# Kernel optimization log

Hardware: AMD Instinct MI355X
Metric: run time of the kernel (lower is better)

## Reference

```python
import jax, jax.numpy as jnp
import numpy as np

EPS = 1e-6
ROPE_THETA = 10000.0


def rms_norm(x, w):
    # x: [..., hd]
    var = jnp.mean(x * x, axis=-1, keepdims=True)
    return x * jax.lax.rsqrt(var + EPS) * w


def apply_rope(x):
    # x: [B, L, nH, hd], rotate-half RoPE over sequence positions
    B, L, nH, hd = x.shape
    half = hd // 2
    inv_freq = 1.0 / (ROPE_THETA ** (jnp.arange(half, dtype=jnp.float32) / half))
    pos = jnp.arange(L, dtype=jnp.float32)
    freqs = pos[:, None] * inv_freq[None, :]          # [L, half]
    cos = jnp.cos(freqs)[None, :, None, :]            # [1, L, 1, half]
    sin = jnp.sin(freqs)[None, :, None, :]
    x1, x2 = x[..., :half], x[..., half:]
    return jnp.concatenate([x1 * cos - x2 * sin, x1 * sin + x2 * cos], axis=-1)


def setup_inputs() -> dict:
    key = jax.random.key(0)
    ks = jax.random.split(key, 5)
    B, H, W, C = 2, 48, 48, 512
    nH, nKV = 8, 4
    hd = C // nH
    s = 0.02
    return {
        "x": jax.random.normal(ks[0], (B, H, W, C), jnp.float32),
        "wq": jax.random.normal(ks[1], (C, C), jnp.float32) * s,
        "wk": jax.random.normal(ks[2], (C, nKV * hd), jnp.float32) * s,
        "wv": jax.random.normal(ks[3], (C, nKV * hd), jnp.float32) * s,
        "wo": jax.random.normal(ks[4], (C, C), jnp.float32) * s,
        "q_norm_w": jnp.ones((hd,), jnp.float32),
        "k_norm_w": jnp.ones((hd,), jnp.float32),
    }


def reference(x, wq, wk, wv, wo, q_norm_w, k_norm_w):
    B, H, W, C = x.shape
    L = H * W
    nH = 8
    hd = C // nH
    nKV = wk.shape[-1] // hd

    xf = x.reshape(B, L, C)
    q = (xf @ wq).reshape(B, L, nH, hd)
    k = (xf @ wk).reshape(B, L, nKV, hd)
    v = (xf @ wv).reshape(B, L, nKV, hd)

    q = apply_rope(rms_norm(q, q_norm_w))
    k = apply_rope(rms_norm(k, k_norm_w))

    q = q.transpose(0, 2, 1, 3)                       # [B, nH, L, hd]
    k = k.transpose(0, 2, 1, 3)                       # [B, nKV, L, hd]
    v = v.transpose(0, 2, 1, 3)
    if nKV < nH:
        rep = nH // nKV
        k = jnp.repeat(k, rep, axis=1)                # repeat_interleave over heads
        v = jnp.repeat(v, rep, axis=1)

    scale = 1.0 / jnp.sqrt(jnp.array(hd, jnp.float32))
    scores = jnp.einsum("bhqd,bhkd->bhqk", q, k) * scale
    attn = jax.nn.softmax(scores, axis=-1)
    out = jnp.einsum("bhqk,bhkd->bhqd", attn, v)      # [B, nH, L, hd]
    out = out.transpose(0, 2, 1, 3).reshape(B, H, W, C)
    return out @ wo
```

## Files before the change

kernel.cpp:

```cpp
#include <hip/hip_runtime.h>
#include <cstdint>
#include <cmath>

typedef float    f32x4  __attribute__((ext_vector_type(4)));
typedef uint32_t u32x4  __attribute__((ext_vector_type(4)));
typedef uint16_t u16x8  __attribute__((ext_vector_type(8)));
typedef __bf16   bf16x8 __attribute__((ext_vector_type(8)));

#define DEVI __device__ __forceinline__

#if __has_builtin(__builtin_amdgcn_exp2f)
DEVI float fast_exp2(float x) { return __builtin_amdgcn_exp2f(x); }
#else
DEVI float fast_exp2(float x) { return exp2f(x); }
#endif

constexpr int L   = 2304;
constexpr int C   = 512;
constexpr int NH  = 8;
constexpr int NKV = 4;
constexpr int HD  = 64;
constexpr int Bn  = 2;
constexpr int M   = Bn * L;
constexpr int NQKV = C + 2 * NKV * HD;
constexpr int NSPLIT = 4;
constexpr int KTILES = 36 / NSPLIT;

DEVI uint16_t f2bf(float f) {
  union { float f; uint32_t u; } v; v.f = f;
  uint32_t u = v.u;
  return (uint16_t)((u + 0x7fffu + ((u >> 16) & 1u)) >> 16);
}
DEVI float bf2f(uint16_t h) {
  union { uint32_t u; float f; } v; v.u = ((uint32_t)h) << 16;
  return v.f;
}
DEVI uint16_t f2h(float f) {
  _Float16 h = (_Float16)f;
  return __builtin_bit_cast(uint16_t, h);
}
DEVI float h2f(uint16_t u) {
  return (float)__builtin_bit_cast(_Float16, u);
}

DEVI bool detect_fp32(const void* qw_raw) {
  return ((const uint16_t*)qw_raw)[0] == 0;
}

DEVI f32x4 mfma_bf16(u32x4 a, u32x4 b, f32x4 c) {
  return __builtin_amdgcn_mfma_f32_16x16x32_bf16(
      __builtin_bit_cast(bf16x8, a), __builtin_bit_cast(bf16x8, b), c, 0, 0, 0);
}

DEVI uint32_t cvt_pk_bf16(float a, float b) {
  uint32_t r;
  asm("v_cvt_pk_bf16_f32 %0, %1, %2" : "=v"(r) : "v"(a), "v"(b));
  return r;
}
DEVI void permlane32_swap(uint32_t& a, uint32_t& b) {
  asm("v_permlane32_swap_b32 %0, %1" : "+v"(a), "+v"(b));
}
DEVI void permlane16_swap(uint32_t& a, uint32_t& b) {
  asm("v_permlane16_swap_b32 %0, %1" : "+v"(a), "+v"(b));
}

DEVI void gld16(const void* g, void* l) {
  __builtin_amdgcn_global_load_lds((const __attribute__((address_space(1))) void*)g,
                                   (__attribute__((address_space(3))) void*)l,
                                   16, 0, 0);
}

__global__ __launch_bounds__(256) void k_prep(
    const void* __restrict__ x,
    const void* __restrict__ wq, const void* __restrict__ wk,
    const void* __restrict__ wv, const void* __restrict__ wo,
    const void* __restrict__ qw_raw,
    uint16_t* __restrict__ xb,
    uint16_t* __restrict__ wqkvT, uint16_t* __restrict__ woT,
    float* __restrict__ rope) {
  const bool f32 = detect_fp32(qw_raw);
  const int bi = blockIdx.x;
  const int t = threadIdx.x;
  if (bi >= 1344) {
    const int idx = (bi - 1344) * 256 + t;
    const int l = idx >> 5, j = idx & 31;
    const float cfreq = -0.41524101186092f;
    const float fj = fast_exp2((float)j * cfreq);
    float sA, cA;
    sincosf((float)l * fj, &sA, &cA);
    rope[idx * 2]     = cA;
    rope[idx * 2 + 1] = sA;
    return;
  }
  if (bi >= 192) {
    const int i = ((bi - 192) * 256 + t) * 8;
    if (f32) {
      const float* xf = (const float*)x;
      const f32x4 v0 = *(const f32x4*)&xf[i];
      const f32x4 v1 = *(const f32x4*)&xf[i + 4];
      u16x8 o;
#pragma unroll
      for (int j = 0; j < 4; ++j) { o[j] = f2bf(v0[j]); o[j + 4] = f2bf(v1[j]); }
      *(u16x8*)&xb[i] = o;
    } else {
      *(u16x8*)&xb[i] = *(const u16x8*)((const uint16_t*)x + i);
    }
    return;
  }
  __shared__ uint16_t tile[64][72];
  const void* src; uint16_t* dst;
  int src_ld, col0, n0, k0;
  if (bi < 128) {
    const int nt = bi & 15, kt = bi >> 4;
    n0 = nt * 64; k0 = kt * 64;
    if (n0 < 512)      { src = wq; src_ld = 512; col0 = n0; }
    else if (n0 < 768) { src = wk; src_ld = 256; col0 = n0 - 512; }
    else               { src = wv; src_ld = 256; col0 = n0 - 768; }
    dst = wqkvT + n0 * 512 + k0;
  } else {
    const int bi2 = bi - 128;
    const int nt = bi2 & 7, kt = bi2 >> 3;
    n0 = nt * 64; k0 = kt * 64;
    src = wo; src_ld = 512; col0 = n0;
    dst = woT + n0 * 512 + k0;
  }
  const int rr = t >> 2, c4 = t & 3;
  if (f32) {
    const float* s32 = (const float*)src;
    for (int cc = c4; cc < 8; cc += 4) {
      const f32x4 v0 = *(const f32x4*)&s32[(k0 + rr) * src_ld + col0 + cc * 8];
      const f32x4 v1 = *(const f32x4*)&s32[(k0 + rr) * src_ld + col0 + cc * 8 + 4];
      for (int j = 0; j < 4; ++j) {
        tile[rr][cc * 8 + j]     = f2bf(v0[j]);
        tile[rr][cc * 8 + j + 4] = f2bf(v1[j]);
      }
    }
  } else {
    const uint16_t* s16 = (const uint16_t*)src;
    for (int cc = c4; cc < 8; cc += 4) {
      const u16x8 v = *(const u16x8*)&s16[(k0 + rr) * src_ld + col0 + cc * 8];
      for (int j = 0; j < 8; ++j) tile[rr][cc * 8 + j] = v[j];
    }
  }
  __syncthreads();
  for (int cc = c4; cc < 8; cc += 4) {
    u16x8 o;
    for (int j = 0; j < 8; ++j) o[j] = tile[cc * 8 + j][rr];
    *(u16x8*)&dst[rr * 512 + cc * 8] = o;
  }
}

DEVI void gemm128x64_core(const uint16_t* __restrict__ A, const uint16_t* __restrict__ Bt,
                          int m0, int n0, uint16_t* As, uint16_t* Bs, f32x4 acc[2][4]) {
  const int t = threadIdx.x;
  const int lane = t & 63, wave = t >> 6;
  const int l15 = lane & 15, quad = lane >> 4;
  const int wm = wave;
#pragma unroll
  for (int i = 0; i < 2; ++i)
#pragma unroll
    for (int j = 0; j < 4; ++j) acc[i][j] = f32x4{0.f, 0.f, 0.f, 0.f};

  for (int k0 = 0; k0 < C; k0 += 64) {
    __syncthreads();
#pragma unroll
    for (int rr = 0; rr < 4; ++rr) {
      const int slotbase = rr * 256 + wave * 64;
      const int slot = slotbase + lane;
      const int row = slot >> 3;
      const int ch = (slot & 7) ^ (row & 7);
      gld16(&A[(m0 + row) * C + k0 + ch * 8], &As[slotbase * 8]);
    }
#pragma unroll
    for (int rr = 0; rr < 2; ++rr) {
      const int slotbase = rr * 256 + wave * 64;
      const int slot = slotbase + lane;
      const int row = slot >> 3;
      const int ch = (slot & 7) ^ (row & 7);
      gld16(&Bt[(n0 + row) * C + k0 + ch * 8], &Bs[slotbase * 8]);
    }
    __syncthreads();
#pragma unroll
    for (int ks = 0; ks < 2; ++ks) {
      const int c = ks * 4 + quad;
      u32x4 af[2], bf[4];
#pragma unroll
      for (int mt = 0; mt < 2; ++mt) {
        const int r = wm * 32 + mt * 16 + l15;
        af[mt] = *(const u32x4*)&As[r * 64 + (c ^ (r & 7)) * 8];
      }
#pragma unroll
      for (int nt = 0; nt < 4; ++nt) {
        const int r = nt * 16 + l15;
        bf[nt] = *(const u32x4*)&Bs[r * 64 + (c ^ (r & 7)) * 8];
      }
#pragma unroll
      for (int mt = 0; mt < 2; ++mt)
#pragma unroll
        for (int nt = 0; nt < 4; ++nt)
          acc[mt][nt] = mfma_bf16(af[mt], bf[nt], acc[mt][nt]);
    }
  }
}

__global__ __launch_bounds__(256, 3) void k_gemm_qkv(
    const uint16_t* __restrict__ xb, const uint16_t* __restrict__ wqkvT,
    uint16_t* __restrict__ q_p, uint16_t* __restrict__ k_p, uint16_t* __restrict__ v_t,
    const void* __restrict__ qw_raw, const void* __restrict__ kw_raw,
    const float* __restrict__ rope) {
  __shared__ uint16_t As[128 * 64], Bs[64 * 64];
  const bool f32 = detect_fp32(qw_raw);
  const int m0 = blockIdx.x * 128, n0 = blockIdx.y * 64;
  f32x4 acc[2][4];
  gemm128x64_core(xb, wqkvT, m0, n0, As, Bs, acc);
  const int t = threadIdx.x, lane = t & 63, wave = t >> 6;
  const int l15 = lane & 15, quad = lane >> 4;
  const int wm = wave;
  const int col0 = n0;

  if (col0 < C + NKV * HD) {
    const bool isq = (col0 < C);
    const void* wr = isq ? qw_raw : kw_raw;
    float w4[4];
#pragma unroll
    for (int nt = 0; nt < 4; ++nt)
      w4[nt] = f32 ? ((const float*)wr)[nt * 16 + l15]
                   : bf2f(((const uint16_t*)wr)[nt * 16 + l15]);
    const float sc = isq ? 0.125f * 1.44269504088896f : 1.0f;
    const int head = isq ? (col0 >> 6) : ((col0 - C) >> 6);
    uint16_t* plane = isq ? q_p : k_p;
    const int nheads = isq ? NH : NKV;
#pragma unroll
    for (int mt = 0; mt < 2; ++mt) {
      const int gm = m0 + wm * 32 + mt * 16 + quad * 4;
      const int b = gm / L;
      const int l = gm - b * L;
      uint16_t* dst = plane + ((b * nheads + head) * L + l) * HD + l15;
#pragma unroll
      for (int r = 0; r < 4; ++r) {
        const float2 cs0 = *(const float2*)&rope[((l + r) * 32 + l15) * 2];
        const float2 cs1 = *(const float2*)&rope[((l + r) * 32 + 16 + l15) * 2];
        float x0 = acc[mt][0][r], x1 = acc[mt][1][r];
        float x2 = acc[mt][2][r], x3 = acc[mt][3][r];
        float ss = x0 * x0 + x1 * x1 + x2 * x2 + x3 * x3;
        ss += __shfl_xor(ss, 1, 64); ss += __shfl_xor(ss, 2, 64);
        ss += __shfl_xor(ss, 4, 64); ss += __shfl_xor(ss, 8, 64);
        const float inv = 1.0f / sqrtf(ss * (1.0f / 64.0f) + 1e-6f);
        x0 *= inv * w4[0]; x1 *= inv * w4[1]; x2 *= inv * w4[2]; x3 *= inv * w4[3];
        dst[r * HD +  0] = f2bf((x0 * cs0.x - x2 * cs0.y) * sc);
        dst[r * HD + 16] = f2bf((x1 * cs1.x - x3 * cs1.y) * sc);
        dst[r * HD + 32] = f2bf((x0 * cs0.y + x2 * cs0.x) * sc);
        dst[r * HD + 48] = f2bf((x1 * cs1.y + x3 * cs1.x) * sc);
      }
    }
  } else {
    const int vh = (col0 - C - NKV * HD) >> 6;
#pragma unroll
    for (int mt = 0; mt < 2; ++mt) {
      const int gm = m0 + wm * 32 + mt * 16 + quad * 4;
      const int b = gm / L;
      const int l = gm - b * L;
#pragma unroll
      for (int nt = 0; nt < 4; ++nt) {
        uint16_t* dst = v_t + ((b * NKV + vh) * HD + nt * 16 + l15) * L + l;
#pragma unroll
        for (int r = 0; r < 4; ++r) dst[r] = f2bf(acc[mt][nt][r]);
      }
    }
  }
}

__global__ __launch_bounds__(256, 3) void k_attn(
    const uint16_t* __restrict__ q_p, const uint16_t* __restrict__ k_p,
    const uint16_t* __restrict__ v_t,
    uint16_t* __restrict__ Ohat, float* __restrict__ lpart) {
  __shared__ uint16_t Ks[2][4096], Vs[2][4096];
  const int t = threadIdx.x, lane = t & 63, wave = t >> 6;
  const int l15 = lane & 15, quad = lane >> 4;

  const int bid = blockIdx.x;
  const int s   = bid / 192;
  const int rem = bid - s * 192;
  const int bkvh = rem / 24;
  const int qg   = rem - bkvh * 24;
  const int b = bkvh >> 2, kvh = bkvh & 3;
  const int u = qg * 4 + wave;
  const int h_local = u / 48;
  const int qt = u - h_local * 48;
  const int bh = b * NH + kvh * 2 + h_local;
  const int q0 = qt * 48;

  const uint16_t* qbase = q_p + (bh * L + q0) * HD;
  const uint16_t* kbase = k_p + (b * NKV + kvh) * L * HD;
  const uint16_t* vbase = v_t + (b * NKV + kvh) * HD * L;
  const int kstart = s * KTILES * 64;

  u32x4 qf[3][2];
#pragma unroll
  for (int mt = 0; mt < 3; ++mt)
#pragma unroll
    for (int ks = 0; ks < 2; ++ks)
      qf[mt][ks] = *(const u32x4*)&qbase[(mt * 16 + l15) * HD + (ks * 4 + quad) * 8];

  f32x4 O[3][4];
  float lp[3];
#pragma unroll
  for (int mt = 0; mt < 3; ++mt) {
#pragma unroll
    for (int nt = 0; nt < 4; ++nt) O[mt][nt] = f32x4{0.f, 0.f, 0.f, 0.f};
    lp[mt] = 0.f;
  }

  auto stageK = [&](int key0, int buf) {
#pragma unroll
    for (int rr = 0; rr < 2; ++rr) {
      const int slotbase = rr * 256 + wave * 64;
      const int slot = slotbase + lane;
      const int row = slot >> 3, cs = slot & 7;
      const int ch = cs ^ (row & 7);
      gld16(&kbase[(key0 + row) * HD + ch * 8], &Ks[buf][slotbase * 8]);
    }
  };
  auto stageV = [&](int key0, int buf) {
#pragma unroll
    for (int rr = 0; rr < 2; ++rr) {
      const int slotbase = rr * 256 + wave * 64;
      const int slot = slotbase + lane;
      const int row = slot >> 3, cs = slot & 7;
      const int ch = cs ^ (row & 7);
      gld16(&vbase[row * L + key0 + ch * 8], &Vs[buf][slotbase * 8]);
    }
  };

  stageK(kstart, 0);
  stageV(kstart, 0);

#pragma unroll 1
  for (int kb = 0; kb < KTILES; ++kb) {
    const int cur = kb & 1;
    __syncthreads();
    if (kb + 1 < KTILES) {
      stageV(kstart + (kb + 1) * 64, cur ^ 1);
      stageK(kstart + (kb + 1) * 64, cur ^ 1);
    }

    u32x4 pa[3][2];

#pragma unroll
    for (int ntp = 0; ntp < 2; ++ntp) {
      f32x4 S[2][3];
#pragma unroll
      for (int ntl = 0; ntl < 2; ++ntl)
#pragma unroll
        for (int mt = 0; mt < 3; ++mt) S[ntl][mt] = f32x4{0.f, 0.f, 0.f, 0.f};
#pragma unroll
      for (int ntl = 0; ntl < 2; ++ntl) {
        const int kr = (ntp * 2 + ntl) * 16 + l15;
#pragma unroll
        for (int dks = 0; dks < 2; ++dks) {
          const int ch = dks * 4 + quad;
          const u32x4 kf = *(const u32x4*)&Ks[cur][(kr * 8 + (ch ^ (kr & 7))) * 8];
          __builtin_amdgcn_s_setprio(1);
#pragma unroll
          for (int mt = 0; mt < 3; ++mt)
            S[ntl][mt] = mfma_bf16(kf, qf[mt][dks], S[ntl][mt]);
          __builtin_amdgcn_s_setprio(0);
        }
      }
      uint32_t P32[2][3][2];
#pragma unroll
      for (int ntl = 0; ntl < 2; ++ntl)
#pragma unroll
        for (int mt = 0; mt < 3; ++mt) {
          const float p0 = fast_exp2(S[ntl][mt][0]);
          const float p1 = fast_exp2(S[ntl][mt][1]);
          const float p2 = fast_exp2(S[ntl][mt][2]);
          const float p3 = fast_exp2(S[ntl][mt][3]);
          lp[mt] += (p0 + p1) + (p2 + p3);
          P32[ntl][mt][0] = cvt_pk_bf16(p0, p1);
          P32[ntl][mt][1] = cvt_pk_bf16(p2, p3);
        }
#pragma unroll
      for (int mt = 0; mt < 3; ++mt)
#pragma unroll
        for (int j2 = 0; j2 < 2; ++j2) {
          uint32_t x = P32[0][mt][j2], y = P32[1][mt][j2];
          permlane32_swap(x, y);
          permlane16_swap(x, y);
          pa[mt][ntp][j2]     = x;
          pa[mt][ntp][2 + j2] = y;
        }
    }

#pragma unroll
    for (int pks = 0; pks < 2; ++pks) {
      const int ch = pks * 4 + quad;
#pragma unroll
      for (int nt = 0; nt < 4; ++nt) {
        const int dr = nt * 16 + l15;
        const u32x4 vf = *(const u32x4*)&Vs[cur][(dr * 8 + (ch ^ (dr & 7))) * 8];
        __builtin_amdgcn_s_setprio(1);
#pragma unroll
        for (int mt = 0; mt < 3; ++mt)
          O[mt][nt] = mfma_bf16(pa[mt][pks], vf, O[mt][nt]);
        __builtin_amdgcn_s_setprio(0);
      }
    }
  }

  const int obase = (s * 16 + bh) * L + q0;
#pragma unroll
  for (int mt = 0; mt < 3; ++mt) {
    float lv = lp[mt];
    lv += __shfl_xor(lv, 16, 64);
    lv += __shfl_xor(lv, 32, 64);
    if (lane < 16) lpart[obase + mt * 16 + lane] = lv;
#pragma unroll
    for (int r = 0; r < 4; ++r) {
      const float rl = 1.0f / __shfl(lv, quad * 4 + r, 64);
      const int row = obase + mt * 16 + quad * 4 + r;
#pragma unroll
      for (int nt = 0; nt < 4; ++nt)
        Ohat[row * HD + nt * 16 + l15] = f2h(O[mt][nt][r] * rl);
    }
  }
}

__global__ __launch_bounds__(256) void k_combine(
    const uint16_t* __restrict__ Ohat, const float* __restrict__ lpart,
    uint16_t* __restrict__ attn) {
  const int idx8 = blockIdx.x * 256 + threadIdx.x;
  const int row = idx8 >> 3, d0 = (idx8 & 7) * 8;
  float o[8] = {0.f, 0.f, 0.f, 0.f, 0.f, 0.f, 0.f, 0.f};
  float l = 0.f;
#pragma unroll
  for (int s = 0; s < NSPLIT; ++s) {
    const float ls = lpart[s * 16 * L + row];
    const u16x8 v = *(const u16x8*)&Ohat[(s * 16 * L + row) * HD + d0];
#pragma unroll
    for (int j = 0; j < 8; ++j) o[j] += h2f(v[j]) * ls;
    l += ls;
  }
  const int bh = row / L, lq = row - bh * L;
  const int b = bh >> 3, h = bh & 7;
  const float rl = 1.0f / l;
  u16x8 ov;
#pragma unroll
  for (int j = 0; j < 8; ++j) ov[j] = f2bf(o[j] * rl);
  *(u16x8*)&attn[(b * L + lq) * C + h * HD + d0] = ov;
}

__global__ __launch_bounds__(256, 3) void k_gemm_out(
    const uint16_t* __restrict__ attn, const uint16_t* __restrict__ woT,
    void* __restrict__ out, const void* __restrict__ qw_raw) {
  __shared__ uint16_t As[128 * 64], Bs[64 * 64];
  const bool f32 = detect_fp32(qw_raw);
  const int m0 = blockIdx.x * 128, n0 = blockIdx.y * 64;
  f32x4 acc[2][4];
  gemm128x64_core(attn, woT, m0, n0, As, Bs, acc);
  const int t = threadIdx.x, lane = t & 63, wave = t >> 6;
  const int l15 = lane & 15, quad = lane >> 4;
  const int wm = wave;
#pragma unroll
  for (int mt = 0; mt < 2; ++mt) {
    const int gm = m0 + wm * 32 + mt * 16 + quad * 4;
#pragma unroll
    for (int nt = 0; nt < 4; ++nt) {
      const int gn = n0 + nt * 16 + l15;
      if (f32) {
        float* o32 = (float*)out;
#pragma unroll
        for (int r = 0; r < 4; ++r) o32[(gm + r) * C + gn] = acc[mt][nt][r];
      } else {
        uint16_t* o16 = (uint16_t*)out;
#pragma unroll
        for (int r = 0; r < 4; ++r) o16[(gm + r) * C + gn] = f2bf(acc[mt][nt][r]);
      }
    }
  }
}

extern "C" void kernel_launch(void* const* d_in, const int* in_sizes, int n_in,
                              void* d_out, int out_size, void* d_ws, size_t ws_size,
                              hipStream_t stream) {
  const void* x  = d_in[0];
  const void* wq = d_in[1];
  const void* wk = d_in[2];
  const void* wv = d_in[3];
  const void* wo = d_in[4];
  const void* qw = d_in[5];
  const void* kw = d_in[6];

  uint16_t* ws = (uint16_t*)d_ws;
  uint16_t* xb    = ws;
  uint16_t* wqkvT = xb    + M * C;
  uint16_t* woT   = wqkvT + 1024 * 512;
  uint16_t* q_p   = woT   + 512 * 512;
  uint16_t* k_p   = q_p + Bn * NH  * L * HD;
  uint16_t* v_t   = k_p + Bn * NKV * L * HD;
  uint16_t* attn  = v_t + Bn * NKV * L * HD;
  uint16_t* Ohat  = attn + M * C;
  float*    lpart = (float*)(Ohat + NSPLIT * 16 * L * HD);
  float*    rope  = lpart + NSPLIT * 16 * L;

  k_prep      <<<dim3(192 + M * C / (256 * 8) + L * 32 / 256), dim3(256), 0, stream>>>(
                  x, wq, wk, wv, wo, qw, xb, wqkvT, woT, rope);
  k_gemm_qkv  <<<dim3(M / 128, NQKV / 64), dim3(256), 0, stream>>>(
                  xb, wqkvT, q_p, k_p, v_t, qw, kw, rope);
  k_attn      <<<dim3(768), dim3(256), 0, stream>>>(q_p, k_p, v_t, Ohat, lpart);
  k_combine   <<<dim3(16 * L * HD / (256 * 8)), dim3(256), 0, stream>>>(Ohat, lpart, attn);
  k_gemm_out  <<<dim3(M / 128, C / 64), dim3(256), 0, stream>>>(attn, woT, d_out, qw);
}
```

Baseline: 127.6 us.

## Fuse split-KV combine into attention kernel via last-arriving-block counter

```diff
diff --git a/kernel.cpp b/kernel.cpp
--- a/kernel.cpp
+++ b/kernel.cpp
@@ -77,10 +77,11 @@
     const void* __restrict__ qw_raw,
     uint16_t* __restrict__ xb,
     uint16_t* __restrict__ wqkvT, uint16_t* __restrict__ woT,
-    float* __restrict__ rope) {
+    float* __restrict__ rope, int* __restrict__ cnt) {
   const bool f32 = detect_fp32(qw_raw);
   const int bi = blockIdx.x;
   const int t = threadIdx.x;
+  if (bi == 0 && t < 192) cnt[t] = 0;
   if (bi >= 1344) {
     const int idx = (bi - 1344) * 256 + t;
     const int l = idx >> 5, j = idx & 31;
@@ -273,8 +274,10 @@
 __global__ __launch_bounds__(256, 3) void k_attn(
     const uint16_t* __restrict__ q_p, const uint16_t* __restrict__ k_p,
     const uint16_t* __restrict__ v_t,
-    uint16_t* __restrict__ Ohat, float* __restrict__ lpart) {
+    uint16_t* __restrict__ Ohat, float* __restrict__ lpart,
+    uint16_t* __restrict__ attn, int* __restrict__ cnt) {
   __shared__ uint16_t Ks[2][4096], Vs[2][4096];
+  __shared__ int oldc;
   const int t = threadIdx.x, lane = t & 63, wave = t >> 6;
   const int l15 = lane & 15, quad = lane >> 4;
 
@@ -424,30 +427,36 @@
         Ohat[row * HD + nt * 16 + l15] = f2h(O[mt][nt][r] * rl);
     }
   }
-}
-
-__global__ __launch_bounds__(256) void k_combine(
-    const uint16_t* __restrict__ Ohat, const float* __restrict__ lpart,
-    uint16_t* __restrict__ attn) {
-  const int idx8 = blockIdx.x * 256 + threadIdx.x;
-  const int row = idx8 >> 3, d0 = (idx8 & 7) * 8;
-  float o[8] = {0.f, 0.f, 0.f, 0.f, 0.f, 0.f, 0.f, 0.f};
-  float l = 0.f;
-#pragma unroll
-  for (int s = 0; s < NSPLIT; ++s) {
-    const float ls = lpart[s * 16 * L + row];
-    const u16x8 v = *(const u16x8*)&Ohat[(s * 16 * L + row) * HD + d0];
-#pragma unroll
-    for (int j = 0; j < 8; ++j) o[j] += h2f(v[j]) * ls;
-    l += ls;
-  }
-  const int bh = row / L, lq = row - bh * L;
-  const int b = bh >> 3, h = bh & 7;
-  const float rl = 1.0f / l;
-  u16x8 ov;
-#pragma unroll
-  for (int j = 0; j < 8; ++j) ov[j] = f2bf(o[j] * rl);
-  *(u16x8*)&attn[(b * L + lq) * C + h * HD + d0] = ov;
+
+  __threadfence();
+  __syncthreads();
+  if (t == 0) oldc = atomicAdd(&cnt[rem], 1);
+  __syncthreads();
+  if (oldc == NSPLIT - 1) {
+    __threadfence();
+    for (int j = t; j < 192 * 8; j += 256) {
+      const int r_loc = j >> 3, d0 = (j & 7) * 8;
+      const int w = r_loc / 48, i = r_loc - w * 48;
+      const int uu = qg * 4 + w;
+      const int hl = uu / 48, qtt = uu - hl * 48;
+      const int row = (b * NH + kvh * 2 + hl) * L + qtt * 48 + i;
+      float o[8] = {0.f, 0.f, 0.f, 0.f, 0.f, 0.f, 0.f, 0.f};
+      float lsum = 0.f;
+#pragma unroll
+      for (int sp = 0; sp < NSPLIT; ++sp) {
+        const float ls = lpart[sp * 16 * L + row];
+        const u16x8 v = *(const u16x8*)&Ohat[(sp * 16 * L + row) * HD + d0];
+#pragma unroll
+        for (int jj = 0; jj < 8; ++jj) o[jj] += h2f(v[jj]) * ls;
+        lsum += ls;
+      }
+      const float rl = 1.0f / lsum;
+      u16x8 ov;
+#pragma unroll
+      for (int jj = 0; jj < 8; ++jj) ov[jj] = f2bf(o[jj] * rl);
+      *(u16x8*)&attn[(b * L + qtt * 48 + i) * C + (kvh * 2 + hl) * HD + d0] = ov;
+    }
+  }
 }
 
 __global__ __launch_bounds__(256, 3) void k_gemm_out(
@@ -502,12 +511,12 @@
   uint16_t* Ohat  = attn + M * C;
   float*    lpart = (float*)(Ohat + NSPLIT * 16 * L * HD);
   float*    rope  = lpart + NSPLIT * 16 * L;
+  int*      cnt   = (int*)(rope + L * 32 * 2);
 
   k_prep      <<<dim3(192 + M * C / (256 * 8) + L * 32 / 256), dim3(256), 0, stream>>>(
-                  x, wq, wk, wv, wo, qw, xb, wqkvT, woT, rope);
+                  x, wq, wk, wv, wo, qw, xb, wqkvT, woT, rope, cnt);
   k_gemm_qkv  <<<dim3(M / 128, NQKV / 64), dim3(256), 0, stream>>>(
                   xb, wqkvT, q_p, k_p, v_t, qw, kw, rope);
-  k_attn      <<<dim3(768), dim3(256), 0, stream>>>(q_p, k_p, v_t, Ohat, lpart);
-  k_combine   <<<dim3(16 * L * HD / (256 * 8)), dim3(256), 0, stream>>>(Ohat, lpart, attn);
+  k_attn      <<<dim3(768), dim3(256), 0, stream>>>(q_p, k_p, v_t, Ohat, lpart, attn, cnt);
   k_gemm_out  <<<dim3(M / 128, C / 64), dim3(256), 0, stream>>>(attn, woT, d_out, qw);
 }
```

Result: slower. 239.8 us (+87.9%).
